# Optimization experiments

Hardware: AMD Instinct MI355X
Metric: run time of the kernel (lower is better)

The kernel has to match this reference:

```python
import jax, jax.numpy as jnp
import numpy as np

B, W, N, F_IN = 2, 8, 10000, 5
E = 80000
H = 128


def setup_inputs() -> dict:
    key = jax.random.key(0)
    ks = jax.random.split(key, 16)
    s = 0.05
    inp = {
        "x": jax.random.normal(ks[0], (B, W, N, F_IN), dtype=jnp.float32),
        "edge_index": jax.random.randint(ks[1], (2, E), 0, N, dtype=jnp.int64),
        # GCN layer 1 (in_features -> hidden) and layer 2 (hidden -> hidden)
        "gcn1_w": jax.random.normal(ks[2], (F_IN, H), dtype=jnp.float32) * s,
        "gcn1_b": jnp.zeros((H,), dtype=jnp.float32),
        "gcn2_w": jax.random.normal(ks[3], (H, H), dtype=jnp.float32) * s,
        "gcn2_b": jnp.zeros((H,), dtype=jnp.float32),
        # LSTM (torch gate order: i, f, g, o)
        "lstm_w_ih": jax.random.normal(ks[4], (4 * H, H), dtype=jnp.float32) * s,
        "lstm_w_hh": jax.random.normal(ks[5], (4 * H, H), dtype=jnp.float32) * s,
        "lstm_b_ih": jnp.zeros((4 * H,), dtype=jnp.float32),
        "lstm_b_hh": jnp.zeros((4 * H,), dtype=jnp.float32),
        # Decoder MLP: H -> H//2 -> 1
        "dec_w1": jax.random.normal(ks[6], (H, H // 2), dtype=jnp.float32) * s,
        "dec_b1": jnp.zeros((H // 2,), dtype=jnp.float32),
        "dec_w2": jax.random.normal(ks[7], (H // 2, 1), dtype=jnp.float32) * s,
        "dec_b2": jnp.zeros((1,), dtype=jnp.float32),
    }
    return inp


def _forward(x, edge_index, gcn1_w, gcn1_b, gcn2_w, gcn2_b,
             lstm_w_ih, lstm_w_hh, lstm_b_ih, lstm_b_hh,
             dec_w1, dec_b1, dec_w2, dec_b2):
    b, w, n, f_in = x.shape
    h_dim = gcn1_w.shape[1]
    # --- GCN normalization (PyG GCNConv default: add self-loops, sym-norm) ---
    loop = jnp.arange(n, dtype=edge_index.dtype)
    src = jnp.concatenate([edge_index[0], loop])
    dst = jnp.concatenate([edge_index[1], loop])
    deg = jnp.zeros((n,), x.dtype).at[dst].add(jnp.float32(1.0))
    dinv = jax.lax.rsqrt(deg)
    norm = dinv[src] * dinv[dst]  # (E+N,)

    def gcn(h, wm, bias):
        # h: (BW, N, Fin) -> (BW, N, H). Transform-then-aggregate (linear op).
        ht = h @ wm                                   # (BW, N, H)
        msg = ht[:, src, :] * norm[None, :, None]      # (BW, E+N, H)
        agg = jnp.zeros_like(ht).at[:, dst, :].add(msg)
        return agg + bias

    xf = x.reshape(b * w, n, f_in)
    h = jax.nn.relu(gcn(xf, gcn1_w, gcn1_b))   # dropout is identity at eval
    h = jax.nn.relu(gcn(h, gcn2_w, gcn2_b))

    # (BW, N, H) -> (B, N, W, H) -> (B*N, W, H): per-node temporal sequences
    h = h.reshape(b, w, n, h_dim).transpose(0, 2, 1, 3).reshape(b * n, w, h_dim)

    # --- single-layer LSTM, keep only last hidden state ---
    def step(carry, xt):
        hp, cp = carry
        gates = xt @ lstm_w_ih.T + hp @ lstm_w_hh.T + lstm_b_ih + lstm_b_hh
        i, f, g, o = jnp.split(gates, 4, axis=-1)
        c = jax.nn.sigmoid(f) * cp + jax.nn.sigmoid(i) * jnp.tanh(g)
        hn = jax.nn.sigmoid(o) * jnp.tanh(c)
        return (hn, c), None

    init = (jnp.zeros((b * n, h_dim), x.dtype), jnp.zeros((b * n, h_dim), x.dtype))
    (h_last, _), _ = jax.lax.scan(step, init, h.transpose(1, 0, 2))  # scan over W

    # --- MLP decoder ---
    d = jax.nn.relu(h_last @ dec_w1 + dec_b1)
    pred = (d @ dec_w2 + dec_b2)[..., 0]
    return pred.reshape(b, n)


def reference(x, edge_index, gcn1_w, gcn1_b, gcn2_w, gcn2_b,
              lstm_w_ih, lstm_w_hh, lstm_b_ih, lstm_b_hh,
              dec_w1, dec_b1, dec_w2, dec_b2):
    return _forward(x, edge_index, gcn1_w, gcn1_b, gcn2_w, gcn2_b,
                    lstm_w_ih, lstm_w_hh, lstm_b_ih, lstm_b_hh,
                    dec_w1, dec_b1, dec_w2, dec_b2)
```

## Files before the change

kernel.cpp:

```cpp
#include <hip/hip_runtime.h>
#include <hip/hip_fp16.h>
#include <cstdint>
#include <cstddef>

#define Bn   2
#define Wn   8
#define Nn   10000
#define Fin  5
#define En   80000
#define Hn   128
#define BWn  (Bn*Wn)
#define ROWS (BWn*Nn)
#define MR   (Bn*Nn)
#define LROWS 32

typedef _Float16 half8 __attribute__((ext_vector_type(8)));
typedef float f32x4 __attribute__((ext_vector_type(4)));

#define LOG2E 1.44269504088896f

__device__ __forceinline__ float fast_sigmoid(float x) {
    return __builtin_amdgcn_rcpf(1.f + __builtin_amdgcn_exp2f(-LOG2E * x));
}
__device__ __forceinline__ float fast_tanh(float x) {
    return fmaf(-2.f, __builtin_amdgcn_rcpf(1.f + __builtin_amdgcn_exp2f(2.f * LOG2E * x)), 1.f);
}

__global__ __launch_bounds__(256) void setup_kernel(
    const int* __restrict__ ei, const float* __restrict__ bih, const float* __restrict__ bhh,
    const float* __restrict__ wih, const float* __restrict__ whh,
    const float* __restrict__ g2w, const float* __restrict__ x,
    int* __restrict__ counts, float* __restrict__ bsum,
    _Float16* __restrict__ wif, _Float16* __restrict__ whf,
    _Float16* __restrict__ g2wt, float* __restrict__ xt) {
    __shared__ float buf[6400];
    const int b = blockIdx.x;
    const int tid = threadIdx.x;
    if (b < 313) {
        int e = b * 256 + tid;
        if (e < En) atomicAdd(&counts[ei[En + e]], 1);
    } else if (b < 315) {
        int i = (b - 313) * 256 + tid;
        if (i < 4 * Hn) bsum[i] = bih[i] + bhh[i];
    } else if (b < 891) {
        int i = (b - 315) * 256 + tid;
        if (i < 131072) {
            int idx = i & 65535;
            int j = idx & 7, lane = (idx >> 3) & 63, kt = (idx >> 9) & 3, ct = idx >> 11;
            int n = ct * 16 + (lane & 15);
            int k = kt * 32 + (lane >> 4) * 8 + j;
            if (i < 65536) wif[idx] = (_Float16)wih[n * 128 + k];
            else           whf[idx] = (_Float16)whh[n * 128 + k];
        } else {
            int j = i - 131072;
            int n = j >> 7, k = j & 127;
            g2wt[j] = (_Float16)g2w[k * Hn + n];
        }
    } else {
        const int n0 = (b - 891) * 80;
        for (int i = tid; i < 6400; i += 256) {
            int s = i / 400, r = i - s * 400;
            int node = r / 5, f = r - node * 5;
            buf[(node * 16 + s) * 5 + f] = x[((size_t)s * Nn + n0) * 5 + r];
        }
        __syncthreads();
        float* dst = xt + (size_t)n0 * 80;
        for (int i = tid; i < 6400; i += 256) dst[i] = buf[i];
    }
}

enum { CHUNK = 10 };
static_assert(CHUNK * 1024 >= Nn, "scan chunk");

__global__ __launch_bounds__(1024) void scan_kernel(
    const int* __restrict__ counts, int* __restrict__ row_ptr,
    int* __restrict__ fill_ptr, float* __restrict__ dinv) {
    __shared__ int sums[1024];
    const int t = threadIdx.x;
    const int base = t * CHUNK;
    int cnt[CHUNK];
    int s = 0;
    #pragma unroll
    for (int i = 0; i < CHUNK; ++i) {
        int idx = base + i;
        int v = (idx < Nn) ? counts[idx] + 1 : 0;
        cnt[i] = v; s += v;
    }
    sums[t] = s;
    __syncthreads();
    for (int off = 1; off < 1024; off <<= 1) {
        int v = (t >= off) ? sums[t - off] : 0;
        __syncthreads();
        sums[t] += v;
        __syncthreads();
    }
    int excl = (t == 0) ? 0 : sums[t - 1];
    #pragma unroll
    for (int i = 0; i < CHUNK; ++i) {
        int idx = base + i;
        if (idx < Nn) {
            row_ptr[idx] = excl;
            fill_ptr[idx] = excl;
            dinv[idx] = rsqrtf((float)cnt[i]);
            excl += cnt[i];
        }
    }
    if (t == 1023) row_ptr[Nn] = excl;
}

__global__ void fill_kernel(const int* __restrict__ ei,
                            const float* __restrict__ dinv,
                            int* fill_ptr, int* __restrict__ col,
                            float* __restrict__ wgt) {
    int i = blockIdx.x * blockDim.x + threadIdx.x;
    if (i < Nn) {
        int p = atomicAdd(&fill_ptr[i], 1);
        col[p] = i;
        wgt[p] = dinv[i] * dinv[i];
    } else if (i < Nn + En) {
        int e = i - Nn;
        int s = ei[e];
        int d = ei[En + e];
        int p = atomicAdd(&fill_ptr[d], 1);
        col[p] = s;
        wgt[p] = dinv[s] * dinv[d];
    }
}

__global__ __launch_bounds__(128) void agg_x_kernel(
    const float* __restrict__ xt, const int* __restrict__ row_ptr,
    const int* __restrict__ col, const float* __restrict__ wgt,
    float* __restrict__ aggx) {
    const int n = blockIdx.x;
    const int t = threadIdx.x;
    const int s = t >> 3, f = t & 7;
    if (f >= Fin) return;
    const int start = row_ptr[n], end = row_ptr[n + 1];
    const int off = s * 5 + f;
    float acc0 = 0.f, acc1 = 0.f;
    int e = start;
    for (; e + 1 < end; e += 2) {
        int c0 = col[e], c1 = col[e + 1];
        float w0 = wgt[e], w1 = wgt[e + 1];
        float v0 = xt[(size_t)c0 * 80 + off];
        float v1 = xt[(size_t)c1 * 80 + off];
        acc0 = fmaf(w0, v0, acc0);
        acc1 = fmaf(w1, v1, acc1);
    }
    if (e < end) acc0 = fmaf(wgt[e], xt[(size_t)col[e] * 80 + off], acc0);
    aggx[(size_t)n * 80 + off] = acc0 + acc1;
}

__global__ __launch_bounds__(256) void gcn2_fused_kernel(
    const float* __restrict__ aggx, const float* __restrict__ w1,
    const float* __restrict__ b1, const _Float16* __restrict__ g2wt,
    _Float16* __restrict__ C) {
    __shared__ __align__(16) _Float16 s_buf[128][136];
    __shared__ _Float16 Bs[128][40];
    const int tid = threadIdx.x;
    const int m0 = blockIdx.x * 128;
    {
        const int rg = tid >> 4;
        const int cg = tid & 15;
        float wreg[Fin][8], breg[8];
        #pragma unroll
        for (int k = 0; k < 8; ++k) breg[k] = b1[cg * 8 + k];
        #pragma unroll
        for (int f = 0; f < Fin; ++f)
            #pragma unroll
            for (int k = 0; k < 8; ++k) wreg[f][k] = w1[f * Hn + cg * 8 + k];
        #pragma unroll
        for (int rr = 0; rr < 8; ++rr) {
            const float* ar = aggx + (size_t)(m0 + rg * 8 + rr) * Fin;
            float a[Fin];
            #pragma unroll
            for (int f = 0; f < Fin; ++f) a[f] = ar[f];
            half8 v;
            #pragma unroll
            for (int k = 0; k < 8; ++k) {
                float s = breg[k];
                #pragma unroll
                for (int f = 0; f < Fin; ++f) s = fmaf(a[f], wreg[f][k], s);
                v[k] = (_Float16)fmaxf(s, 0.f);
            }
            *(half8*)&s_buf[rg * 8 + rr][cg * 8] = v;
        }
    }
    __syncthreads();
    const int wave = tid >> 6, lane = tid & 63;
    const int l = lane & 15, q = lane >> 4;
    const int wm = (wave & 1) * 64, wn = (wave >> 1) * 64;
    f32x4 acc[4][4];
    #pragma unroll
    for (int i = 0; i < 4; ++i)
        #pragma unroll
        for (int j = 0; j < 4; ++j) acc[i][j] = (f32x4){0.f, 0.f, 0.f, 0.f};
    for (int kt = 0; kt < 128; kt += 32) {
        #pragma unroll
        for (int j = 0; j < 2; ++j) {
            int idx = tid + j * 256;
            int r = idx >> 2, c = (idx & 3) * 8;
            *(half8*)&Bs[r][c] = *(const half8*)(g2wt + (size_t)r * 128 + kt + c);
        }
        __syncthreads();
        half8 af[4], bf[4];
        #pragma unroll
        for (int i = 0; i < 4; ++i) af[i] = *(const half8*)&s_buf[wm + i * 16 + l][kt + q * 8];
        #pragma unroll
        for (int j = 0; j < 4; ++j) bf[j] = *(const half8*)&Bs[wn + j * 16 + l][q * 8];
        #pragma unroll
        for (int i = 0; i < 4; ++i)
            #pragma unroll
            for (int j = 0; j < 4; ++j)
                acc[i][j] = __builtin_amdgcn_mfma_f32_16x16x32_f16(
                    af[i], bf[j], acc[i][j], 0, 0, 0);
        __syncthreads();
    }
    #pragma unroll
    for (int j = 0; j < 4; ++j) {
        int ccol = wn + j * 16 + l;
        #pragma unroll
        for (int i = 0; i < 4; ++i)
            #pragma unroll
            for (int r = 0; r < 4; ++r)
                s_buf[wm + i * 16 + q * 4 + r][ccol] = (_Float16)acc[i][j][r];
    }
    __syncthreads();
    const size_t base = (size_t)m0 * 128;
    #pragma unroll
    for (int it = 0; it < 8; ++it) {
        int idx = it * 256 + tid;
        int row = idx >> 4, ch = (idx & 15) * 8;
        *(half8*)(C + base + (size_t)row * 128 + ch) = *(const half8*)&s_buf[row][ch];
    }
}

__global__ __launch_bounds__(256) void gcn_agg2_kernel(
    const _Float16* __restrict__ ht, const int* __restrict__ row_ptr,
    const int* __restrict__ col, const float* __restrict__ wgt,
    const float* __restrict__ bias, _Float16* __restrict__ out) {
    const int n = blockIdx.x;
    const int t = threadIdx.x;
    const int s = t >> 4;
    const int g = (t & 15) * 8;
    const int start = row_ptr[n], end = row_ptr[n + 1];
    const size_t lofs = (size_t)s * Hn + g;
    float acc[8];
    #pragma unroll
    for (int j = 0; j < 8; ++j) acc[j] = 0.f;
    int e = start;
    for (; e + 1 < end; e += 2) {
        const int c0 = col[e], c1 = col[e + 1];
        const float w0 = wgt[e], w1 = wgt[e + 1];
        half8 v0 = *(const half8*)(ht + (size_t)c0 * (BWn * Hn) + lofs);
        half8 v1 = *(const half8*)(ht + (size_t)c1 * (BWn * Hn) + lofs);
        #pragma unroll
        for (int j = 0; j < 8; ++j) {
            acc[j] = fmaf(w0, (float)v0[j], acc[j]);
            acc[j] = fmaf(w1, (float)v1[j], acc[j]);
        }
    }
    if (e < end) {
        const float w = wgt[e];
        half8 v = *(const half8*)(ht + (size_t)col[e] * (BWn * Hn) + lofs);
        #pragma unroll
        for (int j = 0; j < 8; ++j) acc[j] = fmaf(w, (float)v[j], acc[j]);
    }
    half8 o;
    #pragma unroll
    for (int j = 0; j < 8; ++j) o[j] = (_Float16)fmaxf(acc[j] + bias[g + j], 0.f);
    *(half8*)(out + (size_t)n * (BWn * Hn) + lofs) = o;
}

__global__ __launch_bounds__(512, 1) void lstm_fused4_kernel(
    const _Float16* __restrict__ h2, const _Float16* __restrict__ wif,
    const _Float16* __restrict__ whf, const float* __restrict__ bsum,
    _Float16* __restrict__ hf) {
    __shared__ __align__(16) _Float16 x_lds[2][LROWS][144];
    __shared__ __align__(16) _Float16 h_lds[2][LROWS][144];
    const int tid = threadIdx.x;
    const int nw = tid >> 6, lane = tid & 63;
    const int l = lane & 15, q = lane >> 4;
    const int r0 = blockIdx.x * LROWS;
    const int srow = tid >> 4, sch = (tid & 15) * 8;
    const int sgrow = r0 + srow;
    const int sb = (sgrow >= Nn) ? 1 : 0;
    const int sn = sgrow - sb * Nn;
    const _Float16* xbase = h2 + ((size_t)sn * BWn + sb * Wn) * 128 + sch;

    half8 wic[4][4], whc[4][4];
    #pragma unroll
    for (int g = 0; g < 4; ++g) {
        int ct = g * 8 + nw;
        #pragma unroll
        for (int kt = 0; kt < 4; ++kt) {
            wic[g][kt] = *(const half8*)(wif + (((size_t)ct * 4 + kt) * 64 + lane) * 8);
            whc[g][kt] = *(const half8*)(whf + (((size_t)ct * 4 + kt) * 64 + lane) * 8);
        }
    }
    float bias[4];
    #pragma unroll
    for (int g = 0; g < 4; ++g) bias[g] = bsum[g * 128 + nw * 16 + l];
    float c_reg[2][4];
    #pragma unroll
    for (int i = 0; i < 2; ++i)
        #pragma unroll
        for (int r = 0; r < 4; ++r) c_reg[i][r] = 0.f;

    *(half8*)&x_lds[0][srow][sch] = *(const half8*)(xbase);
    __syncthreads();

    for (int t = 0; t < Wn; ++t) {
        half8 xv = {0, 0, 0, 0, 0, 0, 0, 0};
        if (t + 1 < Wn) xv = *(const half8*)(xbase + (size_t)(t + 1) * 128);

        f32x4 acc[2][4];
        #pragma unroll
        for (int i = 0; i < 2; ++i)
            #pragma unroll
            for (int g = 0; g < 4; ++g)
                acc[i][g] = (f32x4){bias[g], bias[g], bias[g], bias[g]};

        #pragma unroll
        for (int kt = 0; kt < 4; ++kt) {
            half8 af[2];
            #pragma unroll
            for (int i = 0; i < 2; ++i)
                af[i] = *(const half8*)&x_lds[t & 1][i * 16 + l][kt * 32 + q * 8];
            #pragma unroll
            for (int i = 0; i < 2; ++i)
                #pragma unroll
                for (int g = 0; g < 4; ++g)
                    acc[i][g] = __builtin_amdgcn_mfma_f32_16x16x32_f16(
                        af[i], wic[g][kt], acc[i][g], 0, 0, 0);
        }
        if (t > 0) {
            #pragma unroll
            for (int kt = 0; kt < 4; ++kt) {
                half8 af[2];
                #pragma unroll
                for (int i = 0; i < 2; ++i)
                    af[i] = *(const half8*)&h_lds[t & 1][i * 16 + l][kt * 32 + q * 8];
                #pragma unroll
                for (int i = 0; i < 2; ++i)
                    #pragma unroll
                    for (int g = 0; g < 4; ++g)
                        acc[i][g] = __builtin_amdgcn_mfma_f32_16x16x32_f16(
                            af[i], whc[g][kt], acc[i][g], 0, 0, 0);
            }
        }

        #pragma unroll
        for (int i = 0; i < 2; ++i) {
            #pragma unroll
            for (int r = 0; r < 4; ++r) {
                float si = fast_sigmoid(acc[i][0][r]);
                float sf = fast_sigmoid(acc[i][1][r]);
                float tg = fast_tanh(acc[i][2][r]);
                float so = fast_sigmoid(acc[i][3][r]);
                float cn = sf * c_reg[i][r] + si * tg;
                c_reg[i][r] = cn;
                h_lds[(t + 1) & 1][i * 16 + q * 4 + r][nw * 16 + l] =
                    (_Float16)(so * fast_tanh(cn));
            }
        }
        if (t + 1 < Wn) *(half8*)&x_lds[(t + 1) & 1][srow][sch] = xv;
        __syncthreads();
    }
    *(half8*)(hf + (size_t)sgrow * 128 + sch) = *(const half8*)&h_lds[0][srow][sch];
}

__global__ __launch_bounds__(256) void decoder_kernel(
    const _Float16* __restrict__ h, const float* __restrict__ w1,
    const float* __restrict__ b1, const float* __restrict__ w2,
    const float* __restrict__ b2, float* __restrict__ out) {
    const int wave = threadIdx.x >> 6;
    const int lane = threadIdx.x & 63;
    const int row = blockIdx.x * 4 + wave;
    if (row >= MR) return;
    const _Float16* hr = h + (size_t)row * Hn;
    float d = b1[lane];
    #pragma unroll 8
    for (int k = 0; k < Hn; ++k) d = fmaf((float)hr[k], w1[k * 64 + lane], d);
    d = fmaxf(d, 0.f);
    float p = d * w2[lane];
    #pragma unroll
    for (int off = 32; off; off >>= 1) p += __shfl_down(p, off);
    if (lane == 0) out[row] = p + b2[0];
}


extern "C" void kernel_launch(void* const* d_in, const int* in_sizes, int n_in,
                              void* d_out, int out_size, void* d_ws, size_t ws_size,
                              hipStream_t stream) {
    const float* x   = (const float*)d_in[0];
    const int*   ei  = (const int*)d_in[1];
    const float* g1w = (const float*)d_in[2];
    const float* g1b = (const float*)d_in[3];
    const float* g2w = (const float*)d_in[4];
    const float* g2b = (const float*)d_in[5];
    const float* wih = (const float*)d_in[6];
    const float* whh = (const float*)d_in[7];
    const float* bih = (const float*)d_in[8];
    const float* bhh = (const float*)d_in[9];
    const float* dw1 = (const float*)d_in[10];
    const float* db1 = (const float*)d_in[11];
    const float* dw2 = (const float*)d_in[12];
    const float* db2 = (const float*)d_in[13];
    float* out = (float*)d_out;

    char* p = (char*)d_ws;
    auto alloc = [&](size_t bytes) {
        char* r = p;
        p += (bytes + 255) & ~(size_t)255;
        return r;
    };
    int*      counts   = (int*)     alloc(Nn * 4);
    int*      row_ptr  = (int*)     alloc((Nn + 1) * 4);
    int*      fill_ptr = (int*)     alloc((Nn + 1) * 4);
    float*    dinv     = (float*)   alloc(Nn * 4);
    float*    bsum     = (float*)   alloc(4 * Hn * 4);
    int*      col      = (int*)     alloc((En + Nn) * 4);
    float*    wgt      = (float*)   alloc((En + Nn) * 4);
    _Float16* wif      = (_Float16*)alloc(512 * 128 * 2);
    _Float16* whf      = (_Float16*)alloc(512 * 128 * 2);
    _Float16* g2wt     = (_Float16*)alloc(128 * 128 * 2);
    float*    xt       = (float*)   alloc((size_t)Nn * 80 * 4);
    float*    aggx     = (float*)   alloc((size_t)ROWS * Fin * 4);
    _Float16* htf      = (_Float16*)alloc((size_t)ROWS * Hn * 2);
    _Float16* h2f      = (_Float16*)alloc((size_t)ROWS * Hn * 2);
    _Float16* hf       = (_Float16*)alloc((size_t)MR * Hn * 2);

    hipMemsetAsync(counts, 0, Nn * 4, stream);

    setup_kernel<<<1016, 256, 0, stream>>>(ei, bih, bhh, wih, whh, g2w, x,
                                           counts, bsum, wif, whf, g2wt, xt);
    scan_kernel<<<1, 1024, 0, stream>>>(counts, row_ptr, fill_ptr, dinv);
    fill_kernel<<<(Nn + En + 255) / 256, 256, 0, stream>>>(ei, dinv, fill_ptr, col, wgt);

    agg_x_kernel<<<Nn, 128, 0, stream>>>(xt, row_ptr, col, wgt, aggx);

    gcn2_fused_kernel<<<ROWS / 128, 256, 0, stream>>>(aggx, g1w, g1b, g2wt, htf);

    gcn_agg2_kernel<<<Nn, 256, 0, stream>>>(htf, row_ptr, col, wgt, g2b, h2f);

    lstm_fused4_kernel<<<MR / LROWS, 512, 0, stream>>>(h2f, wif, whf, bsum, hf);

    decoder_kernel<<<(MR + 3) / 4, 256, 0, stream>>>(hf, dw1, db1, dw2, db2, out);
}
```

Baseline: 276.3 us.

## Fuse decoder MLP into LSTM kernel and split GCN aggregation blocks

```diff
diff --git a/kernel.cpp b/kernel.cpp
--- a/kernel.cpp
+++ b/kernel.cpp
@@ -235,13 +235,13 @@
     }
 }
 
-__global__ __launch_bounds__(256) void gcn_agg2_kernel(
+__global__ __launch_bounds__(128) void gcn_agg2_kernel(
     const _Float16* __restrict__ ht, const int* __restrict__ row_ptr,
     const int* __restrict__ col, const float* __restrict__ wgt,
     const float* __restrict__ bias, _Float16* __restrict__ out) {
     const int n = blockIdx.x;
     const int t = threadIdx.x;
-    const int s = t >> 4;
+    const int s = blockIdx.y * 8 + (t >> 4);
     const int g = (t & 15) * 8;
     const int start = row_ptr[n], end = row_ptr[n + 1];
     const size_t lofs = (size_t)s * Hn + g;
@@ -249,18 +249,22 @@
     #pragma unroll
     for (int j = 0; j < 8; ++j) acc[j] = 0.f;
     int e = start;
-    for (; e + 1 < end; e += 2) {
-        const int c0 = col[e], c1 = col[e + 1];
-        const float w0 = wgt[e], w1 = wgt[e + 1];
+    for (; e + 3 < end; e += 4) {
+        const int c0 = col[e], c1 = col[e + 1], c2 = col[e + 2], c3 = col[e + 3];
+        const float w0 = wgt[e], w1 = wgt[e + 1], w2 = wgt[e + 2], w3 = wgt[e + 3];
         half8 v0 = *(const half8*)(ht + (size_t)c0 * (BWn * Hn) + lofs);
         half8 v1 = *(const half8*)(ht + (size_t)c1 * (BWn * Hn) + lofs);
+        half8 v2 = *(const half8*)(ht + (size_t)c2 * (BWn * Hn) + lofs);
+        half8 v3 = *(const half8*)(ht + (size_t)c3 * (BWn * Hn) + lofs);
         #pragma unroll
         for (int j = 0; j < 8; ++j) {
             acc[j] = fmaf(w0, (float)v0[j], acc[j]);
             acc[j] = fmaf(w1, (float)v1[j], acc[j]);
-        }
-    }
-    if (e < end) {
+            acc[j] = fmaf(w2, (float)v2[j], acc[j]);
+            acc[j] = fmaf(w3, (float)v3[j], acc[j]);
+        }
+    }
+    for (; e < end; ++e) {
         const float w = wgt[e];
         half8 v = *(const half8*)(ht + (size_t)col[e] * (BWn * Hn) + lofs);
         #pragma unroll
@@ -272,10 +276,12 @@
     *(half8*)(out + (size_t)n * (BWn * Hn) + lofs) = o;
 }
 
-__global__ __launch_bounds__(512, 1) void lstm_fused4_kernel(
+__global__ __launch_bounds__(512, 1) void lstm_fused5_kernel(
     const _Float16* __restrict__ h2, const _Float16* __restrict__ wif,
     const _Float16* __restrict__ whf, const float* __restrict__ bsum,
-    _Float16* __restrict__ hf) {
+    const float* __restrict__ dw1, const float* __restrict__ db1,
+    const float* __restrict__ dw2, const float* __restrict__ db2,
+    float* __restrict__ out) {
     __shared__ __align__(16) _Float16 x_lds[2][LROWS][144];
     __shared__ __align__(16) _Float16 h_lds[2][LROWS][144];
     const int tid = threadIdx.x;
@@ -367,26 +373,26 @@
         if (t + 1 < Wn) *(half8*)&x_lds[(t + 1) & 1][srow][sch] = xv;
         __syncthreads();
     }
-    *(half8*)(hf + (size_t)sgrow * 128 + sch) = *(const half8*)&h_lds[0][srow][sch];
-}
-
-__global__ __launch_bounds__(256) void decoder_kernel(
-    const _Float16* __restrict__ h, const float* __restrict__ w1,
-    const float* __restrict__ b1, const float* __restrict__ w2,
-    const float* __restrict__ b2, float* __restrict__ out) {
-    const int wave = threadIdx.x >> 6;
-    const int lane = threadIdx.x & 63;
-    const int row = blockIdx.x * 4 + wave;
-    if (row >= MR) return;
-    const _Float16* hr = h + (size_t)row * Hn;
-    float d = b1[lane];
-    #pragma unroll 8
-    for (int k = 0; k < Hn; ++k) d = fmaf((float)hr[k], w1[k * 64 + lane], d);
-    d = fmaxf(d, 0.f);
-    float p = d * w2[lane];
-    #pragma unroll
-    for (int off = 32; off; off >>= 1) p += __shfl_down(p, off);
-    if (lane == 0) out[row] = p + b2[0];
+
+    _Float16* dw1s = &x_lds[0][0][0];
+    for (int i = tid; i < 8192; i += 512) dw1s[i] = (_Float16)dw1[i];
+    __syncthreads();
+    const float bd1 = db1[lane];
+    const float wd2 = dw2[lane];
+    const float bd2 = db2[0];
+    #pragma unroll
+    for (int rr = 0; rr < 4; ++rr) {
+        const int row = nw * 4 + rr;
+        float d = bd1;
+        #pragma unroll 4
+        for (int k = 0; k < Hn; ++k)
+            d = fmaf((float)h_lds[0][row][k], (float)dw1s[k * 64 + lane], d);
+        d = fmaxf(d, 0.f);
+        float pv = d * wd2;
+        #pragma unroll
+        for (int off = 32; off; off >>= 1) pv += __shfl_down(pv, off);
+        if (lane == 0) out[r0 + row] = pv + bd2;
+    }
 }
 
 
@@ -429,7 +435,6 @@
     float*    aggx     = (float*)   alloc((size_t)ROWS * Fin * 4);
     _Float16* htf      = (_Float16*)alloc((size_t)ROWS * Hn * 2);
     _Float16* h2f      = (_Float16*)alloc((size_t)ROWS * Hn * 2);
-    _Float16* hf       = (_Float16*)alloc((size_t)MR * Hn * 2);
 
     hipMemsetAsync(counts, 0, Nn * 4, stream);
 
@@ -442,9 +447,8 @@
 
     gcn2_fused_kernel<<<ROWS / 128, 256, 0, stream>>>(aggx, g1w, g1b, g2wt, htf);
 
-    gcn_agg2_kernel<<<Nn, 256, 0, stream>>>(htf, row_ptr, col, wgt, g2b, h2f);
-
-    lstm_fused4_kernel<<<MR / LROWS, 512, 0, stream>>>(h2f, wif, whf, bsum, hf);
-
-    decoder_kernel<<<(MR + 3) / 4, 256, 0, stream>>>(hf, dw1, db1, dw2, db2, out);
-}
+    gcn_agg2_kernel<<<dim3(Nn, 2), 128, 0, stream>>>(htf, row_ptr, col, wgt, g2b, h2f);
+
+    lstm_fused5_kernel<<<MR / LROWS, 512, 0, stream>>>(
+        h2f, wif, whf, bsum, dw1, db1, dw2, db2, out);
+}
```

Measured after the change: 267.7 us. 1.03x faster.
